# Performance work log

Hardware: AMD Instinct MI355X
Metric: run time of the kernel (lower is better)

Reference implementation:

```python
import jax, jax.numpy as jnp
import numpy as np

N_ATOMS = 2_000_000
N_STRUCT = 16_384

def _leaky(x):
    return jnp.where(x >= 0, x, 0.01 * x)

def setup_inputs() -> dict:
    key = jax.random.key(0)
    ks = jax.random.split(key, 16)
    atom_prop = jax.random.normal(ks[0], (N_ATOMS, 3), dtype=jnp.float32)
    pos = jax.random.normal(ks[1], (N_ATOMS, 3), dtype=jnp.float32)
    # well-conditioned cells: identity + small perturbation (must be invertible)
    cell = jnp.eye(3, dtype=jnp.float32)[None] + 0.1 * jax.random.normal(ks[2], (N_STRUCT, 3, 3), dtype=jnp.float32)
    batch = jnp.sort(jax.random.randint(ks[3], (N_ATOMS,), 0, N_STRUCT, dtype=jnp.int32))
    s = 0.1
    w0 = s * jax.random.normal(ks[4], (3, 3), dtype=jnp.float32); b0 = jnp.zeros((3,), jnp.float32)
    w1 = jnp.eye(3, dtype=jnp.float32); b1 = jnp.zeros((3,), jnp.float32)
    w1n = jnp.eye(3, dtype=jnp.float32); b1n = jnp.zeros((3,), jnp.float32)
    w2a = s * jax.random.normal(ks[5], (32, 90), dtype=jnp.float32); b2a = jnp.zeros((32,), jnp.float32)
    w2b = s * jax.random.normal(ks[6], (16, 32), dtype=jnp.float32); b2b = jnp.zeros((16,), jnp.float32)
    w2c = s * jax.random.normal(ks[7], (6, 16), dtype=jnp.float32); b2c = jnp.zeros((6,), jnp.float32)
    return dict(atom_prop=atom_prop, pos=pos, cell=cell, batch=batch,
                w0=w0, b0=b0, w1=w1, b1=b1, w1n=w1n, b1n=b1n,
                w2a=w2a, b2a=b2a, w2b=w2b, b2b=b2b, w2c=w2c, b2c=b2c)

def reference(atom_prop, pos, cell, batch, w0, b0, w1, b1, w1n, b1n, w2a, b2a, w2b, b2b, w2c, b2c):
    # cell outer product features: [S,9] -> [S,81], gathered per atom
    cr = cell.reshape(-1, 9)
    cell_ravel = (cr[:, :, None] * cr[:, None, :]).reshape(-1, 81)[batch]  # [N,81]
    cell_inv = jnp.linalg.inv(cell)  # [S,3,3]
    frac_pos = jnp.einsum('nd,nde->ne', pos, cell_inv[batch])  # [N,3]
    threshold = frac_pos - jnp.floor(frac_pos) - 0.5
    atom_prop3 = _leaky(atom_prop @ w0.T + b0)
    t1 = jax.nn.relu(threshold @ w1.T + b1) * atom_prop3
    t2 = jax.nn.relu((-threshold) @ w1n.T + b1n) * atom_prop3
    h = jnp.concatenate((atom_prop, t1, t2, cell_ravel), axis=1)  # [N,90]
    h = jax.nn.relu(h @ w2a.T + b2a)
    h = _leaky(h @ w2b.T + b2b)
    h = h @ w2c.T + b2c  # [N,6]
    stress = jax.ops.segment_sum(h, batch, num_segments=N_STRUCT)  # [S,6]
    return stress
```

## Files before the change

### kernel.cpp

```cpp
#include <hip/hip_runtime.h>
#include <limits.h>

#define BLOCK 256
#define CHUNK 2
#define SPAN  64

typedef float v2f __attribute__((ext_vector_type(2)));

__device__ __forceinline__ v2f pk_fma(v2f a, v2f b, v2f c) {
    return __builtin_elementwise_fma(a, b, c);
}
__device__ __forceinline__ float leaky_(float x){ return x >= 0.f ? x : 0.01f*x; }

#define L_W2AI   0
#define L_W2BT   320
#define L_W2CT   832
#define L_B2B    960
#define L_B2C    976
#define L_W013   984
#define WTAB_SZ  1024
#define L_ACC    1024
#define L_TOT    (1024 + SPAN*6)

__global__ void prep_kernel(const float* __restrict__ cell,
                            const float* __restrict__ w2a,
                            const float* __restrict__ b2a,
                            const float* __restrict__ w2b,
                            const float* __restrict__ w2c,
                            const float* __restrict__ w0, const float* __restrict__ b0,
                            const float* __restrict__ w1, const float* __restrict__ b1,
                            const float* __restrict__ w1n, const float* __restrict__ b1n,
                            const float* __restrict__ b2b, const float* __restrict__ b2c,
                            float* __restrict__ ci_out,
                            float* __restrict__ cc_out,
                            float* __restrict__ wtab,
                            float* __restrict__ out_zero,
                            int S)
{
    int gid = blockIdx.x * blockDim.x + threadIdx.x;

    if (gid < S * 6) out_zero[gid] = 0.f;

    if (gid < 320) {
        int kp = gid / 20, idx = gid % 20;
        int j = idx >> 1, h = idx & 1;
        wtab[L_W2AI + gid] = (idx < 18) ? w2a[(2*kp + h)*90 + j] : 0.f;
    } else if (gid < 832) {
        int t = gid - 320; int k = t >> 4, m = t & 15;
        wtab[gid] = w2b[m*32 + k];
    } else if (gid < 960) {
        int t = gid - 832; int m = t >> 3, p = t & 7;
        wtab[gid] = (p < 6) ? w2c[p*16 + m] : 0.f;
    } else if (gid < 976) {
        wtab[gid] = b2b[gid - 960];
    } else if (gid < 984) {
        int t = gid - 976; wtab[gid] = (t < 6) ? b2c[t] : 0.f;
    } else if (gid < 1024) {
        int t = gid - 984;
        if (t < 36) {
            int mat = t / 12, rr = t % 12, r = rr >> 2, c = rr & 3;
            const float* W = (mat == 0) ? w0 : (mat == 1) ? w1 : w1n;
            const float* B = (mat == 0) ? b0 : (mat == 1) ? b1 : b1n;
            wtab[gid] = (c < 3) ? W[r*3 + c] : B[r];
        } else wtab[gid] = 0.f;
    }

    int s = gid >> 5;
    if (s >= S) return;
    int k = gid & 31;

    float cr[9];
    #pragma unroll
    for (int j = 0; j < 9; j++) cr[j] = cell[s*9 + j];

    if (k == 0) {
        float a=cr[0],b=cr[1],c=cr[2],d=cr[3],e=cr[4],f=cr[5],g=cr[6],h=cr[7],i=cr[8];
        float A = e*i - f*h;
        float B = f*g - d*i;
        float C = d*h - e*g;
        float det = a*A + b*B + c*C;
        float r = 1.0f / det;
        float* o = ci_out + s*12;
        o[0] = A*r;         o[1] = (c*h - b*i)*r; o[2] = (b*f - c*e)*r;
        o[3] = B*r;         o[4] = (a*i - c*g)*r; o[5] = (c*d - a*f)*r;
        o[6] = C*r;         o[7] = (b*g - a*h)*r; o[8] = (a*e - b*d)*r;
        o[9] = 0.f; o[10] = 0.f; o[11] = 0.f;
    }

    float acc = b2a[k];
    const float* wr = w2a + k*90 + 9;
    #pragma unroll
    for (int j1 = 0; j1 < 9; j1++) {
        float c1 = cr[j1];
        #pragma unroll
        for (int j2 = 0; j2 < 9; j2++)
            acc = fmaf(c1 * cr[j2], wr[j1*9 + j2], acc);
    }
    cc_out[s*32 + k] = acc;
}

__global__ __launch_bounds__(BLOCK)
void main_kernel(const float* __restrict__ atom_prop,
                 const float* __restrict__ pos,
                 const int*   __restrict__ batch,
                 const float* __restrict__ ci_ws,
                 const float* __restrict__ cc_ws,
                 const float* __restrict__ wtab,
                 float* __restrict__ out,
                 int N, int S)
{
    __shared__ float lds[L_TOT];
    int tid = threadIdx.x;

    ((float4*)lds)[tid] = ((const float4*)wtab)[tid];
    for (int t = tid; t < SPAN*6; t += BLOCK) lds[L_ACC + t] = 0.f;

    long long blk_base = (long long)blockIdx.x * BLOCK * CHUNK;
    int s0 = batch[(blk_base < N) ? blk_base : (N - 1)];

    __syncthreads();

    long long base = blk_base + (long long)tid * CHUNK;
    bool any = (base < N);

    int   sv[CHUNK];
    float PX[CHUNK], PY[CHUNK], PZ[CHUNK];
    float AX[CHUNK], AY[CHUNK], AZ[CHUNK];

    if (any && base + CHUNK <= N) {
        int2 bb = *(const int2*)(batch + base);
        sv[0] = bb.x; sv[1] = bb.y;
        const float2* pp = (const float2*)(pos + 3*base);
        float2 p0 = pp[0], p1 = pp[1], p2 = pp[2];
        PX[0]=p0.x; PY[0]=p0.y; PZ[0]=p1.x;
        PX[1]=p1.y; PY[1]=p2.x; PZ[1]=p2.y;
        const float2* ap = (const float2*)(atom_prop + 3*base);
        float2 a0 = ap[0], a1 = ap[1], a2 = ap[2];
        AX[0]=a0.x; AY[0]=a0.y; AZ[0]=a1.x;
        AX[1]=a1.y; AY[1]=a2.x; AZ[1]=a2.y;
    } else {
        #pragma unroll
        for (int t = 0; t < CHUNK; t++) {
            long long i = base + t;
            bool ok = any && (i < N);
            sv[t] = ok ? batch[i] : -1;
            PX[t] = ok ? pos[3*i]   : 0.f;
            PY[t] = ok ? pos[3*i+1] : 0.f;
            PZ[t] = ok ? pos[3*i+2] : 0.f;
            AX[t] = ok ? atom_prop[3*i]   : 0.f;
            AY[t] = ok ? atom_prop[3*i+1] : 0.f;
            AZ[t] = ok ? atom_prop[3*i+2] : 0.f;
        }
    }

    v2f h2[CHUNK][9];
    {
        const float4* q0 = (const float4*)(lds + L_W013);
        const float4* q1 = (const float4*)(lds + L_W013 + 12);
        const float4* q2 = (const float4*)(lds + L_W013 + 24);
        int   cur_s = -1;
        float ci[9];
        #pragma unroll
        for (int t = 0; t < CHUNK; t++) {
            int s = sv[t];
            if (s < 0) {
                #pragma unroll
                for (int j = 0; j < 9; j++) h2[t][j] = 0.f;
                continue;
            }
            if (s != cur_s) {
                cur_s = s;
                const float4* cip = (const float4*)(ci_ws + (size_t)s*12);
                float4 c0 = cip[0], c1 = cip[1], c2 = cip[2];
                ci[0]=c0.x; ci[1]=c0.y; ci[2]=c0.z; ci[3]=c0.w;
                ci[4]=c1.x; ci[5]=c1.y; ci[6]=c1.z; ci[7]=c1.w;
                ci[8]=c2.x;
            }
            float px = PX[t], py = PY[t], pz = PZ[t];
            float ax = AX[t], ay = AY[t], az = AZ[t];

            float f0 = fmaf(px, ci[0], fmaf(py, ci[3], pz*ci[6]));
            float f1 = fmaf(px, ci[1], fmaf(py, ci[4], pz*ci[7]));
            float f2 = fmaf(px, ci[2], fmaf(py, ci[5], pz*ci[8]));
            float t0 = f0 - floorf(f0) - 0.5f;
            float t1 = f1 - floorf(f1) - 0.5f;
            float t2 = f2 - floorf(f2) - 0.5f;

            h2[t][0].x = h2[t][0].y = ax;
            h2[t][1].x = h2[t][1].y = ay;
            h2[t][2].x = h2[t][2].y = az;
            #pragma unroll
            for (int r = 0; r < 3; r++) {
                float4 a0 = q0[r], a1 = q1[r], a2 = q2[r];
                float ap3 = leaky_(fmaf(ax, a0.x, fmaf(ay, a0.y, fmaf(az, a0.z, a0.w))));
                float d1  = fmaf(t0, a1.x, fmaf(t1, a1.y, fmaf(t2, a1.z, a1.w)));
                float d2  = a2.w - fmaf(t0, a2.x, fmaf(t1, a2.y, t2*a2.z));
                float v1 = fmaxf(d1, 0.f) * ap3;
                float v2 = fmaxf(d2, 0.f) * ap3;
                h2[t][3+r].x = h2[t][3+r].y = v1;
                h2[t][6+r].x = h2[t][6+r].y = v2;
            }
        }
    }

    v2f vv[CHUNK][8];
    {
        const v2f* b2b2 = (const v2f*)(lds + L_B2B);
        #pragma unroll
        for (int t = 0; t < CHUNK; t++)
            #pragma unroll
            for (int m2 = 0; m2 < 8; m2++) vv[t][m2] = b2b2[m2];
    }

    const float* ccp[CHUNK];
    #pragma unroll
    for (int t = 0; t < CHUNK; t++) {
        int s = sv[t] < 0 ? 0 : sv[t];
        ccp[t] = cc_ws + (size_t)s*32;
    }

    float4 c4n[CHUNK];
    #pragma unroll
    for (int t = 0; t < CHUNK; t++) c4n[t] = *(const float4*)(ccp[t]);

    #pragma unroll
    for (int kb = 0; kb < 8; kb++) {
        float4 c4[CHUNK];
        #pragma unroll
        for (int t = 0; t < CHUNK; t++) c4[t] = c4n[t];
        if (kb < 7) {
            #pragma unroll
            for (int t = 0; t < CHUNK; t++) c4n[t] = *(const float4*)(ccp[t] + (kb+1)*4);
        }

        #pragma unroll
        for (int h = 0; h < 2; h++) {
            int kp = 2*kb + h;
            const v2f* wI  = (const v2f*)(lds + L_W2AI + kp*20);
            const v2f* wb0 = (const v2f*)(lds + L_W2BT + (2*kp)*16);
            const v2f* wb1 = (const v2f*)(lds + L_W2BT + (2*kp+1)*16);
            #pragma unroll
            for (int t = 0; t < CHUNK; t++) {
                v2f u2;
                u2.x = h ? c4[t].z : c4[t].x;
                u2.y = h ? c4[t].w : c4[t].y;
                #pragma unroll
                for (int j = 0; j < 9; j++) u2 = pk_fma(h2[t][j], wI[j], u2);
                v2f zero = 0.f;
                u2 = __builtin_elementwise_max(u2, zero);
                v2f ux; ux.x = u2.x; ux.y = u2.x;
                v2f uy; uy.x = u2.y; uy.y = u2.y;
                #pragma unroll
                for (int m2 = 0; m2 < 8; m2++) {
                    vv[t][m2] = pk_fma(ux, wb0[m2], vv[t][m2]);
                    vv[t][m2] = pk_fma(uy, wb1[m2], vv[t][m2]);
                }
            }
        }
    }

    {
        v2f zero = 0.f, small = 0.01f;
        #pragma unroll
        for (int t = 0; t < CHUNK; t++)
            #pragma unroll
            for (int m2 = 0; m2 < 8; m2++) {
                v2f mx = __builtin_elementwise_max(vv[t][m2], zero);
                v2f mn = __builtin_elementwise_min(vv[t][m2], zero);
                vv[t][m2] = pk_fma(mn, small, mx);
            }
    }

    v2f oo[CHUNK][3];
    {
        const v2f* b2c2 = (const v2f*)(lds + L_B2C);
        #pragma unroll
        for (int t = 0; t < CHUNK; t++)
            #pragma unroll
            for (int p2 = 0; p2 < 3; p2++) oo[t][p2] = b2c2[p2];
    }
    #pragma unroll
    for (int m2 = 0; m2 < 8; m2++) {
        const v2f* wc0 = (const v2f*)(lds + L_W2CT + (2*m2)*8);
        const v2f* wc1 = (const v2f*)(lds + L_W2CT + (2*m2+1)*8);
        #pragma unroll
        for (int t = 0; t < CHUNK; t++) {
            v2f vm = vv[t][m2];
            v2f a; a.x = vm.x; a.y = vm.x;
            v2f b; b.x = vm.y; b.y = vm.y;
            #pragma unroll
            for (int p2 = 0; p2 < 3; p2++)
                oo[t][p2] = pk_fma(a, wc0[p2], pk_fma(b, wc1[p2], oo[t][p2]));
        }
    }

    const int SENT = INT_MAX;
    int fs;
    float fin[6];
    {
        int sA = sv[0], sB = sv[1];
        if (sA < 0) {
            fs = SENT;
            #pragma unroll
            for (int p = 0; p < 6; p++) fin[p] = 0.f;
        } else if (sB == sA) {
            fs = sA;
            fin[0] = oo[0][0].x + oo[1][0].x; fin[1] = oo[0][0].y + oo[1][0].y;
            fin[2] = oo[0][1].x + oo[1][1].x; fin[3] = oo[0][1].y + oo[1][1].y;
            fin[4] = oo[0][2].x + oo[1][2].x; fin[5] = oo[0][2].y + oo[1][2].y;
        } else {
            float v0[6] = {oo[0][0].x, oo[0][0].y, oo[0][1].x, oo[0][1].y, oo[0][2].x, oo[0][2].y};
            int idx = sA - s0;
            if (idx >= 0 && idx < SPAN) {
                #pragma unroll
                for (int p = 0; p < 6; p++) atomicAdd(&lds[L_ACC + idx*6 + p], v0[p]);
            } else {
                #pragma unroll
                for (int p = 0; p < 6; p++) atomicAdd(out + (size_t)sA*6 + p, v0[p]);
            }
            if (sB >= 0) {
                fs = sB;
                fin[0] = oo[1][0].x; fin[1] = oo[1][0].y;
                fin[2] = oo[1][1].x; fin[3] = oo[1][1].y;
                fin[4] = oo[1][2].x; fin[5] = oo[1][2].y;
            } else {
                fs = SENT;
                #pragma unroll
                for (int p = 0; p < 6; p++) fin[p] = 0.f;
            }
        }
    }

    int lane = tid & 63;
    #pragma unroll
    for (int d = 1; d < 64; d <<= 1) {
        int ks = __shfl_up(fs, d);
        bool pred = (lane >= d) && (ks == fs);
        #pragma unroll
        for (int p = 0; p < 6; p++) {
            float vp = __shfl_up(fin[p], d);
            fin[p] += pred ? vp : 0.f;
        }
    }
    {
        int sn = __shfl_down(fs, 1);
        bool tail = (lane == 63) || (sn != fs);
        if (tail && fs != SENT) {
            int idx = fs - s0;
            if (idx >= 0 && idx < SPAN) {
                #pragma unroll
                for (int p = 0; p < 6; p++) atomicAdd(&lds[L_ACC + idx*6 + p], fin[p]);
            } else {
                #pragma unroll
                for (int p = 0; p < 6; p++) atomicAdd(out + (size_t)fs*6 + p, fin[p]);
            }
        }
    }

    __syncthreads();

    for (int e = tid; e < SPAN*6; e += BLOCK) {
        int idx = e / 6, p = e - idx*6;
        int sg = s0 + idx;
        float v = lds[L_ACC + e];
        if (sg < S && v != 0.f) atomicAdd(out + (size_t)sg*6 + p, v);
    }
}

extern "C" void kernel_launch(void* const* d_in, const int* in_sizes, int n_in,
                              void* d_out, int out_size, void* d_ws, size_t ws_size,
                              hipStream_t stream)
{
    const float* atom_prop = (const float*)d_in[0];
    const float* pos       = (const float*)d_in[1];
    const float* cell      = (const float*)d_in[2];
    const int*   batch     = (const int*)  d_in[3];
    const float* w0  = (const float*)d_in[4];
    const float* b0  = (const float*)d_in[5];
    const float* w1  = (const float*)d_in[6];
    const float* b1  = (const float*)d_in[7];
    const float* w1n = (const float*)d_in[8];
    const float* b1n = (const float*)d_in[9];
    const float* w2a = (const float*)d_in[10];
    const float* b2a = (const float*)d_in[11];
    const float* w2b = (const float*)d_in[12];
    const float* b2b = (const float*)d_in[13];
    const float* w2c = (const float*)d_in[14];
    const float* b2c = (const float*)d_in[15];

    int N = in_sizes[3];
    int S = in_sizes[2] / 9;

    float* out   = (float*)d_out;
    float* ci_ws = (float*)d_ws;
    float* cc_ws = ci_ws + (size_t)S*12;
    float* wtab  = cc_ws + (size_t)S*32;

    int prep_threads = S * 32;
    prep_kernel<<<(prep_threads + 255)/256, 256, 0, stream>>>(
        cell, w2a, b2a, w2b, w2c, w0, b0, w1, b1, w1n, b1n, b2b, b2c,
        ci_ws, cc_ws, wtab, out, S);

    long long total_threads = ((long long)N + CHUNK - 1) / CHUNK;
    int grid = (int)((total_threads + BLOCK - 1) / BLOCK);
    main_kernel<<<grid, BLOCK, 0, stream>>>(atom_prop, pos, batch,
                                            ci_ws, cc_ws, wtab, out, N, S);
}
```

Measured before the change: 172.7 us.

## Make main kernel persistent with grid-stride tiles and vectorized LDS weight loads

The main kernel becomes a persistent grid of at most 1792 blocks that loop over 512-atom tiles, so the weight table is loaded into LDS once per block instead of once per tile. Each tile now adds two barriers to reset the LDS accumulator. The cc_ws prefetch is moved ahead of the first-layer compute, and weights are read from LDS as float4 vectors. Launch bounds now request 7 blocks per CU, which may limit registers and force spills.

```diff
diff --git a/kernel.cpp b/kernel.cpp
--- a/kernel.cpp
+++ b/kernel.cpp
@@ -4,6 +4,7 @@
 #define BLOCK 256
 #define CHUNK 2
 #define SPAN  64
+#define PERSIST_BLOCKS 1792
 
 typedef float v2f __attribute__((ext_vector_type(2)));
 
@@ -99,7 +100,7 @@
     cc_out[s*32 + k] = acc;
 }
 
-__global__ __launch_bounds__(BLOCK)
+__global__ __launch_bounds__(BLOCK, 7)
 void main_kernel(const float* __restrict__ atom_prop,
                  const float* __restrict__ pos,
                  const int*   __restrict__ batch,
@@ -107,263 +108,292 @@
                  const float* __restrict__ cc_ws,
                  const float* __restrict__ wtab,
                  float* __restrict__ out,
-                 int N, int S)
+                 int N, int S, int ntiles)
 {
     __shared__ float lds[L_TOT];
     int tid = threadIdx.x;
 
     ((float4*)lds)[tid] = ((const float4*)wtab)[tid];
-    for (int t = tid; t < SPAN*6; t += BLOCK) lds[L_ACC + t] = 0.f;
-
-    long long blk_base = (long long)blockIdx.x * BLOCK * CHUNK;
-    int s0 = batch[(blk_base < N) ? blk_base : (N - 1)];
-
-    __syncthreads();
-
-    long long base = blk_base + (long long)tid * CHUNK;
-    bool any = (base < N);
-
-    int   sv[CHUNK];
-    float PX[CHUNK], PY[CHUNK], PZ[CHUNK];
-    float AX[CHUNK], AY[CHUNK], AZ[CHUNK];
-
-    if (any && base + CHUNK <= N) {
-        int2 bb = *(const int2*)(batch + base);
-        sv[0] = bb.x; sv[1] = bb.y;
-        const float2* pp = (const float2*)(pos + 3*base);
-        float2 p0 = pp[0], p1 = pp[1], p2 = pp[2];
-        PX[0]=p0.x; PY[0]=p0.y; PZ[0]=p1.x;
-        PX[1]=p1.y; PY[1]=p2.x; PZ[1]=p2.y;
-        const float2* ap = (const float2*)(atom_prop + 3*base);
-        float2 a0 = ap[0], a1 = ap[1], a2 = ap[2];
-        AX[0]=a0.x; AY[0]=a0.y; AZ[0]=a1.x;
-        AX[1]=a1.y; AY[1]=a2.x; AZ[1]=a2.y;
-    } else {
+
+    for (int tile = blockIdx.x; tile < ntiles; tile += gridDim.x) {
+        long long blk_base = (long long)tile * (BLOCK * CHUNK);
+        int s0 = batch[(blk_base < N) ? blk_base : (N - 1)];
+
+        __syncthreads();
+        for (int t = tid; t < SPAN*6; t += BLOCK) lds[L_ACC + t] = 0.f;
+        __syncthreads();
+
+        long long base = blk_base + (long long)tid * CHUNK;
+        bool any = (base < N);
+
+        int   sv[CHUNK];
+        float PX[CHUNK], PY[CHUNK], PZ[CHUNK];
+        float AX[CHUNK], AY[CHUNK], AZ[CHUNK];
+
+        if (any && base + CHUNK <= N) {
+            int2 bb = *(const int2*)(batch + base);
+            sv[0] = bb.x; sv[1] = bb.y;
+            const float2* pp = (const float2*)(pos + 3*base);
+            float2 p0 = pp[0], p1 = pp[1], p2 = pp[2];
+            PX[0]=p0.x; PY[0]=p0.y; PZ[0]=p1.x;
+            PX[1]=p1.y; PY[1]=p2.x; PZ[1]=p2.y;
+            const float2* ap = (const float2*)(atom_prop + 3*base);
+            float2 a0 = ap[0], a1 = ap[1], a2 = ap[2];
+            AX[0]=a0.x; AY[0]=a0.y; AZ[0]=a1.x;
+            AX[1]=a1.y; AY[1]=a2.x; AZ[1]=a2.y;
+        } else {
+            #pragma unroll
+            for (int t = 0; t < CHUNK; t++) {
+                long long i = base + t;
+                bool ok = any && (i < N);
+                sv[t] = ok ? batch[i] : -1;
+                PX[t] = ok ? pos[3*i]   : 0.f;
+                PY[t] = ok ? pos[3*i+1] : 0.f;
+                PZ[t] = ok ? pos[3*i+2] : 0.f;
+                AX[t] = ok ? atom_prop[3*i]   : 0.f;
+                AY[t] = ok ? atom_prop[3*i+1] : 0.f;
+                AZ[t] = ok ? atom_prop[3*i+2] : 0.f;
+            }
+        }
+
+        const float* ccp[CHUNK];
         #pragma unroll
         for (int t = 0; t < CHUNK; t++) {
-            long long i = base + t;
-            bool ok = any && (i < N);
-            sv[t] = ok ? batch[i] : -1;
-            PX[t] = ok ? pos[3*i]   : 0.f;
-            PY[t] = ok ? pos[3*i+1] : 0.f;
-            PZ[t] = ok ? pos[3*i+2] : 0.f;
-            AX[t] = ok ? atom_prop[3*i]   : 0.f;
-            AY[t] = ok ? atom_prop[3*i+1] : 0.f;
-            AZ[t] = ok ? atom_prop[3*i+2] : 0.f;
-        }
-    }
-
-    v2f h2[CHUNK][9];
-    {
-        const float4* q0 = (const float4*)(lds + L_W013);
-        const float4* q1 = (const float4*)(lds + L_W013 + 12);
-        const float4* q2 = (const float4*)(lds + L_W013 + 24);
-        int   cur_s = -1;
-        float ci[9];
-        #pragma unroll
-        for (int t = 0; t < CHUNK; t++) {
-            int s = sv[t];
-            if (s < 0) {
-                #pragma unroll
-                for (int j = 0; j < 9; j++) h2[t][j] = 0.f;
-                continue;
-            }
-            if (s != cur_s) {
-                cur_s = s;
-                const float4* cip = (const float4*)(ci_ws + (size_t)s*12);
-                float4 c0 = cip[0], c1 = cip[1], c2 = cip[2];
-                ci[0]=c0.x; ci[1]=c0.y; ci[2]=c0.z; ci[3]=c0.w;
-                ci[4]=c1.x; ci[5]=c1.y; ci[6]=c1.z; ci[7]=c1.w;
-                ci[8]=c2.x;
-            }
-            float px = PX[t], py = PY[t], pz = PZ[t];
-            float ax = AX[t], ay = AY[t], az = AZ[t];
-
-            float f0 = fmaf(px, ci[0], fmaf(py, ci[3], pz*ci[6]));
-            float f1 = fmaf(px, ci[1], fmaf(py, ci[4], pz*ci[7]));
-            float f2 = fmaf(px, ci[2], fmaf(py, ci[5], pz*ci[8]));
-            float t0 = f0 - floorf(f0) - 0.5f;
-            float t1 = f1 - floorf(f1) - 0.5f;
-            float t2 = f2 - floorf(f2) - 0.5f;
-
-            h2[t][0].x = h2[t][0].y = ax;
-            h2[t][1].x = h2[t][1].y = ay;
-            h2[t][2].x = h2[t][2].y = az;
-            #pragma unroll
-            for (int r = 0; r < 3; r++) {
-                float4 a0 = q0[r], a1 = q1[r], a2 = q2[r];
-                float ap3 = leaky_(fmaf(ax, a0.x, fmaf(ay, a0.y, fmaf(az, a0.z, a0.w))));
-                float d1  = fmaf(t0, a1.x, fmaf(t1, a1.y, fmaf(t2, a1.z, a1.w)));
-                float d2  = a2.w - fmaf(t0, a2.x, fmaf(t1, a2.y, t2*a2.z));
-                float v1 = fmaxf(d1, 0.f) * ap3;
-                float v2 = fmaxf(d2, 0.f) * ap3;
-                h2[t][3+r].x = h2[t][3+r].y = v1;
-                h2[t][6+r].x = h2[t][6+r].y = v2;
-            }
-        }
-    }
-
-    v2f vv[CHUNK][8];
-    {
-        const v2f* b2b2 = (const v2f*)(lds + L_B2B);
-        #pragma unroll
-        for (int t = 0; t < CHUNK; t++)
-            #pragma unroll
-            for (int m2 = 0; m2 < 8; m2++) vv[t][m2] = b2b2[m2];
-    }
-
-    const float* ccp[CHUNK];
-    #pragma unroll
-    for (int t = 0; t < CHUNK; t++) {
-        int s = sv[t] < 0 ? 0 : sv[t];
-        ccp[t] = cc_ws + (size_t)s*32;
-    }
-
-    float4 c4n[CHUNK];
-    #pragma unroll
-    for (int t = 0; t < CHUNK; t++) c4n[t] = *(const float4*)(ccp[t]);
-
-    #pragma unroll
-    for (int kb = 0; kb < 8; kb++) {
-        float4 c4[CHUNK];
-        #pragma unroll
-        for (int t = 0; t < CHUNK; t++) c4[t] = c4n[t];
-        if (kb < 7) {
-            #pragma unroll
-            for (int t = 0; t < CHUNK; t++) c4n[t] = *(const float4*)(ccp[t] + (kb+1)*4);
-        }
-
-        #pragma unroll
-        for (int h = 0; h < 2; h++) {
-            int kp = 2*kb + h;
-            const v2f* wI  = (const v2f*)(lds + L_W2AI + kp*20);
-            const v2f* wb0 = (const v2f*)(lds + L_W2BT + (2*kp)*16);
-            const v2f* wb1 = (const v2f*)(lds + L_W2BT + (2*kp+1)*16);
+            int s = sv[t] < 0 ? 0 : sv[t];
+            ccp[t] = cc_ws + (size_t)s*32;
+        }
+        float4 c4n[CHUNK];
+        #pragma unroll
+        for (int t = 0; t < CHUNK; t++) c4n[t] = *(const float4*)(ccp[t]);
+
+        v2f h2[CHUNK][9];
+        {
+            const float4* q0 = (const float4*)(lds + L_W013);
+            const float4* q1 = (const float4*)(lds + L_W013 + 12);
+            const float4* q2 = (const float4*)(lds + L_W013 + 24);
+            int   cur_s = -1;
+            float ci[9];
             #pragma unroll
             for (int t = 0; t < CHUNK; t++) {
-                v2f u2;
-                u2.x = h ? c4[t].z : c4[t].x;
-                u2.y = h ? c4[t].w : c4[t].y;
-                #pragma unroll
-                for (int j = 0; j < 9; j++) u2 = pk_fma(h2[t][j], wI[j], u2);
-                v2f zero = 0.f;
-                u2 = __builtin_elementwise_max(u2, zero);
-                v2f ux; ux.x = u2.x; ux.y = u2.x;
-                v2f uy; uy.x = u2.y; uy.y = u2.y;
+                int s = sv[t];
+                if (s < 0) {
+                    #pragma unroll
+                    for (int j = 0; j < 9; j++) h2[t][j] = 0.f;
+                    continue;
+                }
+                if (s != cur_s) {
+                    cur_s = s;
+                    const float4* cip = (const float4*)(ci_ws + (size_t)s*12);
+                    float4 c0 = cip[0], c1 = cip[1], c2 = cip[2];
+                    ci[0]=c0.x; ci[1]=c0.y; ci[2]=c0.z; ci[3]=c0.w;
+                    ci[4]=c1.x; ci[5]=c1.y; ci[6]=c1.z; ci[7]=c1.w;
+                    ci[8]=c2.x;
+                }
+                float px = PX[t], py = PY[t], pz = PZ[t];
+                float ax = AX[t], ay = AY[t], az = AZ[t];
+
+                float f0 = fmaf(px, ci[0], fmaf(py, ci[3], pz*ci[6]));
+                float f1 = fmaf(px, ci[1], fmaf(py, ci[4], pz*ci[7]));
+                float f2 = fmaf(px, ci[2], fmaf(py, ci[5], pz*ci[8]));
+                float t0 = f0 - floorf(f0) - 0.5f;
+                float t1 = f1 - floorf(f1) - 0.5f;
+                float t2 = f2 - floorf(f2) - 0.5f;
+
+                h2[t][0].x = h2[t][0].y = ax;
+                h2[t][1].x = h2[t][1].y = ay;
+                h2[t][2].x = h2[t][2].y = az;
+                #pragma unroll
+                for (int r = 0; r < 3; r++) {
+                    float4 a0 = q0[r], a1 = q1[r], a2 = q2[r];
+                    float ap3 = leaky_(fmaf(ax, a0.x, fmaf(ay, a0.y, fmaf(az, a0.z, a0.w))));
+                    float d1  = fmaf(t0, a1.x, fmaf(t1, a1.y, fmaf(t2, a1.z, a1.w)));
+                    float d2  = a2.w - fmaf(t0, a2.x, fmaf(t1, a2.y, t2*a2.z));
+                    float v1 = fmaxf(d1, 0.f) * ap3;
+                    float v2 = fmaxf(d2, 0.f) * ap3;
+                    h2[t][3+r].x = h2[t][3+r].y = v1;
+                    h2[t][6+r].x = h2[t][6+r].y = v2;
+                }
+            }
+        }
+
+        v2f vv[CHUNK][8];
+        {
+            const v2f* b2b2 = (const v2f*)(lds + L_B2B);
+            #pragma unroll
+            for (int t = 0; t < CHUNK; t++)
+                #pragma unroll
+                for (int m2 = 0; m2 < 8; m2++) vv[t][m2] = b2b2[m2];
+        }
+
+        #pragma unroll
+        for (int kb = 0; kb < 8; kb++) {
+            float4 c4[CHUNK];
+            #pragma unroll
+            for (int t = 0; t < CHUNK; t++) c4[t] = c4n[t];
+            if (kb < 7) {
+                #pragma unroll
+                for (int t = 0; t < CHUNK; t++) c4n[t] = *(const float4*)(ccp[t] + (kb+1)*4);
+            }
+
+            #pragma unroll
+            for (int h = 0; h < 2; h++) {
+                int kp = 2*kb + h;
+                const float4* wI4  = (const float4*)(lds + L_W2AI + kp*20);
+                float4 wq0 = wI4[0], wq1 = wI4[1], wq2 = wI4[2], wq3 = wI4[3], wq4 = wI4[4];
+                v2f wj[9];
+                wj[0].x=wq0.x; wj[0].y=wq0.y;  wj[1].x=wq0.z; wj[1].y=wq0.w;
+                wj[2].x=wq1.x; wj[2].y=wq1.y;  wj[3].x=wq1.z; wj[3].y=wq1.w;
+                wj[4].x=wq2.x; wj[4].y=wq2.y;  wj[5].x=wq2.z; wj[5].y=wq2.w;
+                wj[6].x=wq3.x; wj[6].y=wq3.y;  wj[7].x=wq3.z; wj[7].y=wq3.w;
+                wj[8].x=wq4.x; wj[8].y=wq4.y;
+
+                const float4* wb04 = (const float4*)(lds + L_W2BT + (2*kp)*16);
+                const float4* wb14 = (const float4*)(lds + L_W2BT + (2*kp+1)*16);
+                float4 b0q[4], b1q[4];
+                #pragma unroll
+                for (int q = 0; q < 4; q++) { b0q[q] = wb04[q]; b1q[q] = wb14[q]; }
+                v2f wb0v[8], wb1v[8];
+                #pragma unroll
+                for (int q = 0; q < 4; q++) {
+                    wb0v[2*q].x   = b0q[q].x; wb0v[2*q].y   = b0q[q].y;
+                    wb0v[2*q+1].x = b0q[q].z; wb0v[2*q+1].y = b0q[q].w;
+                    wb1v[2*q].x   = b1q[q].x; wb1v[2*q].y   = b1q[q].y;
+                    wb1v[2*q+1].x = b1q[q].z; wb1v[2*q+1].y = b1q[q].w;
+                }
+
+                #pragma unroll
+                for (int t = 0; t < CHUNK; t++) {
+                    v2f u2;
+                    u2.x = h ? c4[t].z : c4[t].x;
+                    u2.y = h ? c4[t].w : c4[t].y;
+                    #pragma unroll
+                    for (int j = 0; j < 9; j++) u2 = pk_fma(h2[t][j], wj[j], u2);
+                    v2f zero = 0.f;
+                    u2 = __builtin_elementwise_max(u2, zero);
+                    v2f ux; ux.x = u2.x; ux.y = u2.x;
+                    v2f uy; uy.x = u2.y; uy.y = u2.y;
+                    #pragma unroll
+                    for (int m2 = 0; m2 < 8; m2++) {
+                        vv[t][m2] = pk_fma(ux, wb0v[m2], vv[t][m2]);
+                        vv[t][m2] = pk_fma(uy, wb1v[m2], vv[t][m2]);
+                    }
+                }
+            }
+        }
+
+        {
+            v2f zero = 0.f, small = 0.01f;
+            #pragma unroll
+            for (int t = 0; t < CHUNK; t++)
                 #pragma unroll
                 for (int m2 = 0; m2 < 8; m2++) {
-                    vv[t][m2] = pk_fma(ux, wb0[m2], vv[t][m2]);
-                    vv[t][m2] = pk_fma(uy, wb1[m2], vv[t][m2]);
-                }
-            }
-        }
-    }
-
-    {
-        v2f zero = 0.f, small = 0.01f;
-        #pragma unroll
-        for (int t = 0; t < CHUNK; t++)
-            #pragma unroll
-            for (int m2 = 0; m2 < 8; m2++) {
-                v2f mx = __builtin_elementwise_max(vv[t][m2], zero);
-                v2f mn = __builtin_elementwise_min(vv[t][m2], zero);
-                vv[t][m2] = pk_fma(mn, small, mx);
-            }
-    }
-
-    v2f oo[CHUNK][3];
-    {
-        const v2f* b2c2 = (const v2f*)(lds + L_B2C);
-        #pragma unroll
-        for (int t = 0; t < CHUNK; t++)
-            #pragma unroll
-            for (int p2 = 0; p2 < 3; p2++) oo[t][p2] = b2c2[p2];
-    }
-    #pragma unroll
-    for (int m2 = 0; m2 < 8; m2++) {
-        const v2f* wc0 = (const v2f*)(lds + L_W2CT + (2*m2)*8);
-        const v2f* wc1 = (const v2f*)(lds + L_W2CT + (2*m2+1)*8);
-        #pragma unroll
-        for (int t = 0; t < CHUNK; t++) {
-            v2f vm = vv[t][m2];
-            v2f a; a.x = vm.x; a.y = vm.x;
-            v2f b; b.x = vm.y; b.y = vm.y;
-            #pragma unroll
-            for (int p2 = 0; p2 < 3; p2++)
-                oo[t][p2] = pk_fma(a, wc0[p2], pk_fma(b, wc1[p2], oo[t][p2]));
-        }
-    }
-
-    const int SENT = INT_MAX;
-    int fs;
-    float fin[6];
-    {
-        int sA = sv[0], sB = sv[1];
-        if (sA < 0) {
-            fs = SENT;
-            #pragma unroll
-            for (int p = 0; p < 6; p++) fin[p] = 0.f;
-        } else if (sB == sA) {
-            fs = sA;
-            fin[0] = oo[0][0].x + oo[1][0].x; fin[1] = oo[0][0].y + oo[1][0].y;
-            fin[2] = oo[0][1].x + oo[1][1].x; fin[3] = oo[0][1].y + oo[1][1].y;
-            fin[4] = oo[0][2].x + oo[1][2].x; fin[5] = oo[0][2].y + oo[1][2].y;
-        } else {
-            float v0[6] = {oo[0][0].x, oo[0][0].y, oo[0][1].x, oo[0][1].y, oo[0][2].x, oo[0][2].y};
-            int idx = sA - s0;
-            if (idx >= 0 && idx < SPAN) {
-                #pragma unroll
-                for (int p = 0; p < 6; p++) atomicAdd(&lds[L_ACC + idx*6 + p], v0[p]);
+                    v2f mx = __builtin_elementwise_max(vv[t][m2], zero);
+                    v2f mn = __builtin_elementwise_min(vv[t][m2], zero);
+                    vv[t][m2] = pk_fma(mn, small, mx);
+                }
+        }
+
+        v2f oo[CHUNK][3];
+        {
+            const v2f* b2c2 = (const v2f*)(lds + L_B2C);
+            #pragma unroll
+            for (int t = 0; t < CHUNK; t++)
+                #pragma unroll
+                for (int p2 = 0; p2 < 3; p2++) oo[t][p2] = b2c2[p2];
+        }
+        #pragma unroll
+        for (int m2 = 0; m2 < 8; m2++) {
+            const float4* wc04 = (const float4*)(lds + L_W2CT + (2*m2)*8);
+            const float4* wc14 = (const float4*)(lds + L_W2CT + (2*m2+1)*8);
+            float4 c0q0 = wc04[0], c0q1 = wc04[1];
+            float4 c1q0 = wc14[0], c1q1 = wc14[1];
+            v2f wc0v[3], wc1v[3];
+            wc0v[0].x=c0q0.x; wc0v[0].y=c0q0.y; wc0v[1].x=c0q0.z; wc0v[1].y=c0q0.w;
+            wc0v[2].x=c0q1.x; wc0v[2].y=c0q1.y;
+            wc1v[0].x=c1q0.x; wc1v[0].y=c1q0.y; wc1v[1].x=c1q0.z; wc1v[1].y=c1q0.w;
+            wc1v[2].x=c1q1.x; wc1v[2].y=c1q1.y;
+            #pragma unroll
+            for (int t = 0; t < CHUNK; t++) {
+                v2f vm = vv[t][m2];
+                v2f a; a.x = vm.x; a.y = vm.x;
+                v2f b; b.x = vm.y; b.y = vm.y;
+                #pragma unroll
+                for (int p2 = 0; p2 < 3; p2++)
+                    oo[t][p2] = pk_fma(a, wc0v[p2], pk_fma(b, wc1v[p2], oo[t][p2]));
+            }
+        }
+
+        const int SENT = INT_MAX;
+        int fs;
+        float fin[6];
+        {
+            int sA = sv[0], sB = sv[1];
+            if (sA < 0) {
+                fs = SENT;
+                #pragma unroll
+                for (int p = 0; p < 6; p++) fin[p] = 0.f;
+            } else if (sB == sA) {
+                fs = sA;
+                fin[0] = oo[0][0].x + oo[1][0].x; fin[1] = oo[0][0].y + oo[1][0].y;
+                fin[2] = oo[0][1].x + oo[1][1].x; fin[3] = oo[0][1].y + oo[1][1].y;
+                fin[4] = oo[0][2].x + oo[1][2].x; fin[5] = oo[0][2].y + oo[1][2].y;
             } else {
-                #pragma unroll
-                for (int p = 0; p < 6; p++) atomicAdd(out + (size_t)sA*6 + p, v0[p]);
-            }
-            if (sB >= 0) {
-                fs = sB;
-                fin[0] = oo[1][0].x; fin[1] = oo[1][0].y;
-                fin[2] = oo[1][1].x; fin[3] = oo[1][1].y;
-                fin[4] = oo[1][2].x; fin[5] = oo[1][2].y;
-            } else {
-                fs = SENT;
-                #pragma unroll
-                for (int p = 0; p < 6; p++) fin[p] = 0.f;
-            }
-        }
-    }
-
-    int lane = tid & 63;
-    #pragma unroll
-    for (int d = 1; d < 64; d <<= 1) {
-        int ks = __shfl_up(fs, d);
-        bool pred = (lane >= d) && (ks == fs);
-        #pragma unroll
-        for (int p = 0; p < 6; p++) {
-            float vp = __shfl_up(fin[p], d);
-            fin[p] += pred ? vp : 0.f;
-        }
-    }
-    {
-        int sn = __shfl_down(fs, 1);
-        bool tail = (lane == 63) || (sn != fs);
-        if (tail && fs != SENT) {
-            int idx = fs - s0;
-            if (idx >= 0 && idx < SPAN) {
-                #pragma unroll
-                for (int p = 0; p < 6; p++) atomicAdd(&lds[L_ACC + idx*6 + p], fin[p]);
-            } else {
-                #pragma unroll
-                for (int p = 0; p < 6; p++) atomicAdd(out + (size_t)fs*6 + p, fin[p]);
-            }
-        }
-    }
-
-    __syncthreads();
-
-    for (int e = tid; e < SPAN*6; e += BLOCK) {
-        int idx = e / 6, p = e - idx*6;
-        int sg = s0 + idx;
-        float v = lds[L_ACC + e];
-        if (sg < S && v != 0.f) atomicAdd(out + (size_t)sg*6 + p, v);
+                float v0[6] = {oo[0][0].x, oo[0][0].y, oo[0][1].x, oo[0][1].y, oo[0][2].x, oo[0][2].y};
+                int idx = sA - s0;
+                if (idx >= 0 && idx < SPAN) {
+                    #pragma unroll
+                    for (int p = 0; p < 6; p++) atomicAdd(&lds[L_ACC + idx*6 + p], v0[p]);
+                } else {
+                    #pragma unroll
+                    for (int p = 0; p < 6; p++) atomicAdd(out + (size_t)sA*6 + p, v0[p]);
+                }
+                if (sB >= 0) {
+                    fs = sB;
+                    fin[0] = oo[1][0].x; fin[1] = oo[1][0].y;
+                    fin[2] = oo[1][1].x; fin[3] = oo[1][1].y;
+                    fin[4] = oo[1][2].x; fin[5] = oo[1][2].y;
+                } else {
+                    fs = SENT;
+                    #pragma unroll
+                    for (int p = 0; p < 6; p++) fin[p] = 0.f;
+                }
+            }
+        }
+
+        int lane = tid & 63;
+        #pragma unroll
+        for (int d = 1; d < 64; d <<= 1) {
+            int ks = __shfl_up(fs, d);
+            bool pred = (lane >= d) && (ks == fs);
+            #pragma unroll
+            for (int p = 0; p < 6; p++) {
+                float vp = __shfl_up(fin[p], d);
+                fin[p] += pred ? vp : 0.f;
+            }
+        }
+        {
+            int sn = __shfl_down(fs, 1);
+            bool tail = (lane == 63) || (sn != fs);
+            if (tail && fs != SENT) {
+                int idx = fs - s0;
+                if (idx >= 0 && idx < SPAN) {
+                    #pragma unroll
+                    for (int p = 0; p < 6; p++) atomicAdd(&lds[L_ACC + idx*6 + p], fin[p]);
+                } else {
+                    #pragma unroll
+                    for (int p = 0; p < 6; p++) atomicAdd(out + (size_t)fs*6 + p, fin[p]);
+                }
+            }
+        }
+
+        __syncthreads();
+
+        for (int e = tid; e < SPAN*6; e += BLOCK) {
+            int idx = e / 6, p = e - idx*6;
+            int sg = s0 + idx;
+            float v = lds[L_ACC + e];
+            if (sg < S && v != 0.f) atomicAdd(out + (size_t)sg*6 + p, v);
+        }
     }
 }
 
@@ -401,8 +431,9 @@
         cell, w2a, b2a, w2b, w2c, w0, b0, w1, b1, w1n, b1n, b2b, b2c,
         ci_ws, cc_ws, wtab, out, S);
 
-    long long total_threads = ((long long)N + CHUNK - 1) / CHUNK;
-    int grid = (int)((total_threads + BLOCK - 1) / BLOCK);
+    int tile_atoms = BLOCK * CHUNK;
+    int ntiles = (N + tile_atoms - 1) / tile_atoms;
+    int grid = ntiles < PERSIST_BLOCKS ? ntiles : PERSIST_BLOCKS;
     main_kernel<<<grid, BLOCK, 0, stream>>>(atom_prop, pos, batch,
-                                            ci_ws, cc_ws, wtab, out, N, S);
+                                            ci_ws, cc_ws, wtab, out, N, S, ntiles);
 }
```

After: 518.3 us. 3x slower.

## Pack MLP weights as bf16 pairs in LDS and hoist cc loads

Applied to the files above, without the earlier changes.

Stores the w2a, w2b and w2c weight tables in LDS as packed bf16 pairs, unpacked to fp32 with shifts and masks, which roughly halves LDS weight traffic per atom. The per-structure cell-feature loads are moved earlier so their latency overlaps the first-layer compute, and the prep kernel now stages w2a in shared memory. The price is extra ALU work for unpacking and a loss of precision in the weights, which may affect accuracy tolerance.

```diff
diff --git a/kernel.cpp b/kernel.cpp
--- a/kernel.cpp
+++ b/kernel.cpp
@@ -12,15 +12,30 @@
 }
 __device__ __forceinline__ float leaky_(float x){ return x >= 0.f ? x : 0.01f*x; }
 
+__device__ __forceinline__ v2f bfup(unsigned u){
+    v2f r;
+    r.x = __uint_as_float(u << 16);
+    r.y = __uint_as_float(u & 0xffff0000u);
+    return r;
+}
+
+__device__ __forceinline__ unsigned bf1(float x){
+    unsigned u = __float_as_uint(x);
+    return (u + 0x7FFFu + ((u >> 16) & 1u)) >> 16;
+}
+__device__ __forceinline__ float bfpack(float a, float b){
+    return __uint_as_float(bf1(a) | (bf1(b) << 16));
+}
+
 #define L_W2AI   0
-#define L_W2BT   320
-#define L_W2CT   832
-#define L_B2B    960
-#define L_B2C    976
-#define L_W013   984
-#define WTAB_SZ  1024
-#define L_ACC    1024
-#define L_TOT    (1024 + SPAN*6)
+#define L_W2BT   192
+#define L_W2CT   448
+#define L_B2B    512
+#define L_B2C    528
+#define L_W013   536
+#define WTAB_SZ  576
+#define L_ACC    576
+#define L_TOT    (576 + SPAN*6)
 
 __global__ void prep_kernel(const float* __restrict__ cell,
                             const float* __restrict__ w2a,
@@ -37,26 +52,37 @@
                             float* __restrict__ out_zero,
                             int S)
 {
-    int gid = blockIdx.x * blockDim.x + threadIdx.x;
+    __shared__ float sw[2880];
+    int tid = threadIdx.x;
+    int gid = blockIdx.x * blockDim.x + tid;
+
+    #pragma unroll
+    for (int t = 0; t < 3; t++) {
+        int idx = tid + t*256;
+        if (idx < 720) ((float4*)sw)[idx] = ((const float4*)w2a)[idx];
+    }
 
     if (gid < S * 6) out_zero[gid] = 0.f;
 
-    if (gid < 320) {
-        int kp = gid / 20, idx = gid % 20;
-        int j = idx >> 1, h = idx & 1;
-        wtab[L_W2AI + gid] = (idx < 18) ? w2a[(2*kp + h)*90 + j] : 0.f;
-    } else if (gid < 832) {
-        int t = gid - 320; int k = t >> 4, m = t & 15;
-        wtab[gid] = w2b[m*32 + k];
-    } else if (gid < 960) {
-        int t = gid - 832; int m = t >> 3, p = t & 7;
-        wtab[gid] = (p < 6) ? w2c[p*16 + m] : 0.f;
-    } else if (gid < 976) {
-        wtab[gid] = b2b[gid - 960];
-    } else if (gid < 984) {
-        int t = gid - 976; wtab[gid] = (t < 6) ? b2c[t] : 0.f;
-    } else if (gid < 1024) {
-        int t = gid - 984;
+    if (gid < 192) {
+        int kp = gid / 12, j = gid % 12;
+        float a = (j < 9) ? w2a[(2*kp)*90 + j]   : 0.f;
+        float b = (j < 9) ? w2a[(2*kp+1)*90 + j] : 0.f;
+        wtab[L_W2AI + gid] = bfpack(a, b);
+    } else if (gid < 448) {
+        int t = gid - 192; int k = t >> 3, m2 = t & 7;
+        wtab[gid] = bfpack(w2b[(2*m2)*32 + k], w2b[(2*m2+1)*32 + k]);
+    } else if (gid < 512) {
+        int t = gid - 448; int m = t >> 2, p2 = t & 3;
+        float a = (2*p2 < 6)     ? w2c[(2*p2)*16 + m]   : 0.f;
+        float b = (2*p2 + 1 < 6) ? w2c[(2*p2+1)*16 + m] : 0.f;
+        wtab[gid] = bfpack(a, b);
+    } else if (gid < 528) {
+        wtab[gid] = b2b[gid - 512];
+    } else if (gid < 536) {
+        int t = gid - 528; wtab[gid] = (t < 6) ? b2c[t] : 0.f;
+    } else if (gid < 576) {
+        int t = gid - 536;
         if (t < 36) {
             int mat = t / 12, rr = t % 12, r = rr >> 2, c = rr & 3;
             const float* W = (mat == 0) ? w0 : (mat == 1) ? w1 : w1n;
@@ -64,6 +90,8 @@
             wtab[gid] = (c < 3) ? W[r*3 + c] : B[r];
         } else wtab[gid] = 0.f;
     }
+
+    __syncthreads();
 
     int s = gid >> 5;
     if (s >= S) return;
@@ -88,7 +116,7 @@
     }
 
     float acc = b2a[k];
-    const float* wr = w2a + k*90 + 9;
+    const float* wr = sw + k*90 + 9;
     #pragma unroll
     for (int j1 = 0; j1 < 9; j1++) {
         float c1 = cr[j1];
@@ -112,7 +140,7 @@
     __shared__ float lds[L_TOT];
     int tid = threadIdx.x;
 
-    ((float4*)lds)[tid] = ((const float4*)wtab)[tid];
+    if (tid < WTAB_SZ/4) ((float4*)lds)[tid] = ((const float4*)wtab)[tid];
     for (int t = tid; t < SPAN*6; t += BLOCK) lds[L_ACC + t] = 0.f;
 
     long long blk_base = (long long)blockIdx.x * BLOCK * CHUNK;
@@ -153,6 +181,16 @@
         }
     }
 
+    const float* ccp[CHUNK];
+    #pragma unroll
+    for (int t = 0; t < CHUNK; t++) {
+        int s = sv[t] < 0 ? 0 : sv[t];
+        ccp[t] = cc_ws + (size_t)s*32;
+    }
+    float4 c4n[CHUNK];
+    #pragma unroll
+    for (int t = 0; t < CHUNK; t++) c4n[t] = *(const float4*)(ccp[t]);
+
     v2f h2[CHUNK][9];
     {
         const float4* q0 = (const float4*)(lds + L_W013);
@@ -212,17 +250,6 @@
             for (int m2 = 0; m2 < 8; m2++) vv[t][m2] = b2b2[m2];
     }
 
-    const float* ccp[CHUNK];
-    #pragma unroll
-    for (int t = 0; t < CHUNK; t++) {
-        int s = sv[t] < 0 ? 0 : sv[t];
-        ccp[t] = cc_ws + (size_t)s*32;
-    }
-
-    float4 c4n[CHUNK];
-    #pragma unroll
-    for (int t = 0; t < CHUNK; t++) c4n[t] = *(const float4*)(ccp[t]);
-
     #pragma unroll
     for (int kb = 0; kb < 8; kb++) {
         float4 c4[CHUNK];
@@ -236,24 +263,38 @@
         #pragma unroll
         for (int h = 0; h < 2; h++) {
             int kp = 2*kb + h;
-            const v2f* wI  = (const v2f*)(lds + L_W2AI + kp*20);
-            const v2f* wb0 = (const v2f*)(lds + L_W2BT + (2*kp)*16);
-            const v2f* wb1 = (const v2f*)(lds + L_W2BT + (2*kp+1)*16);
+            const uint4* wIq = (const uint4*)(lds + L_W2AI + kp*12);
+            uint4 wqa = wIq[0], wqb = wIq[1];
+            unsigned wqc = ((const unsigned*)(lds + L_W2AI + kp*12))[8];
+            v2f wj[9];
+            wj[0] = bfup(wqa.x); wj[1] = bfup(wqa.y); wj[2] = bfup(wqa.z); wj[3] = bfup(wqa.w);
+            wj[4] = bfup(wqb.x); wj[5] = bfup(wqb.y); wj[6] = bfup(wqb.z); wj[7] = bfup(wqb.w);
+            wj[8] = bfup(wqc);
+
+            const uint4* w0q = (const uint4*)(lds + L_W2BT + (2*kp)*8);
+            const uint4* w1q = (const uint4*)(lds + L_W2BT + (2*kp+1)*8);
+            uint4 p0a = w0q[0], p0b = w0q[1], p1a = w1q[0], p1b = w1q[1];
+            v2f wb0v[8], wb1v[8];
+            wb0v[0]=bfup(p0a.x); wb0v[1]=bfup(p0a.y); wb0v[2]=bfup(p0a.z); wb0v[3]=bfup(p0a.w);
+            wb0v[4]=bfup(p0b.x); wb0v[5]=bfup(p0b.y); wb0v[6]=bfup(p0b.z); wb0v[7]=bfup(p0b.w);
+            wb1v[0]=bfup(p1a.x); wb1v[1]=bfup(p1a.y); wb1v[2]=bfup(p1a.z); wb1v[3]=bfup(p1a.w);
+            wb1v[4]=bfup(p1b.x); wb1v[5]=bfup(p1b.y); wb1v[6]=bfup(p1b.z); wb1v[7]=bfup(p1b.w);
+
             #pragma unroll
             for (int t = 0; t < CHUNK; t++) {
                 v2f u2;
                 u2.x = h ? c4[t].z : c4[t].x;
                 u2.y = h ? c4[t].w : c4[t].y;
                 #pragma unroll
-                for (int j = 0; j < 9; j++) u2 = pk_fma(h2[t][j], wI[j], u2);
+                for (int j = 0; j < 9; j++) u2 = pk_fma(h2[t][j], wj[j], u2);
                 v2f zero = 0.f;
                 u2 = __builtin_elementwise_max(u2, zero);
                 v2f ux; ux.x = u2.x; ux.y = u2.x;
                 v2f uy; uy.x = u2.y; uy.y = u2.y;
                 #pragma unroll
                 for (int m2 = 0; m2 < 8; m2++) {
-                    vv[t][m2] = pk_fma(ux, wb0[m2], vv[t][m2]);
-                    vv[t][m2] = pk_fma(uy, wb1[m2], vv[t][m2]);
+                    vv[t][m2] = pk_fma(ux, wb0v[m2], vv[t][m2]);
+                    vv[t][m2] = pk_fma(uy, wb1v[m2], vv[t][m2]);
                 }
             }
         }
@@ -281,8 +322,10 @@
     }
     #pragma unroll
     for (int m2 = 0; m2 < 8; m2++) {
-        const v2f* wc0 = (const v2f*)(lds + L_W2CT + (2*m2)*8);
-        const v2f* wc1 = (const v2f*)(lds + L_W2CT + (2*m2+1)*8);
+        uint4 q0 = *(const uint4*)(lds + L_W2CT + (2*m2)*4);
+        uint4 q1 = *(const uint4*)(lds + L_W2CT + (2*m2+1)*4);
+        v2f wc0v[3] = {bfup(q0.x), bfup(q0.y), bfup(q0.z)};
+        v2f wc1v[3] = {bfup(q1.x), bfup(q1.y), bfup(q1.z)};
         #pragma unroll
         for (int t = 0; t < CHUNK; t++) {
             v2f vm = vv[t][m2];
@@ -290,7 +333,7 @@
             v2f b; b.x = vm.y; b.y = vm.y;
             #pragma unroll
             for (int p2 = 0; p2 < 3; p2++)
-                oo[t][p2] = pk_fma(a, wc0[p2], pk_fma(b, wc1[p2], oo[t][p2]));
+                oo[t][p2] = pk_fma(a, wc0v[p2], pk_fma(b, wc1v[p2], oo[t][p2]));
         }
     }
 
```

New measurement: 195.4 us. 13.1% more time.
